# Kernel tuning notes

Hardware: AMD Instinct MI355X
Metric: run time of the kernel (lower is better)

The kernel has to match this reference:

```python
import jax, jax.numpy as jnp
import numpy as np

B, D, T, K = 16, 512, 4096, 1024

def setup_inputs() -> dict:
    key = jax.random.key(0)
    kx, kc = jax.random.split(key)
    x = jax.random.normal(kx, (B, D, T), dtype=jnp.float32)
    codebook = jax.random.normal(kc, (K, D), dtype=jnp.float32)
    return {"x": x, "codebook": codebook}

def reference(x, codebook):
    # x: [B, D, T] -> xt: [B, T, D]
    xt = jnp.transpose(x, (0, 2, 1))
    x_sq = jnp.sum(xt * xt, axis=-1, keepdims=True)          # [B, T, 1]
    c_sq = jnp.sum(codebook * codebook, axis=-1)             # [K]
    cross = jnp.einsum('btd,kd->btk', xt, codebook)          # [B, T, K]
    dist = x_sq - 2.0 * cross + c_sq                         # [B, T, K]
    indexes = jnp.argmin(dist, axis=2)                       # [B, T] int
    quantized = codebook[indexes]                            # [B, T, D]
    quantized = jnp.transpose(quantized, (0, 2, 1))          # [B, D, T]
    return quantized, indexes
```

## Files before the change

### kernel.cpp

```cpp
#include <hip/hip_runtime.h>

#define BB 16
#define DD 512
#define TT 4096
#define KK 1024

typedef _Float16 h16;
typedef __attribute__((ext_vector_type(8))) _Float16 half8;
typedef __attribute__((ext_vector_type(4))) float float4v;

#define XTH_OFF 0ull
#define XTL_OFF 67108864ull
#define CBH_OFF 134217728ull
#define CBL_OFF 135266304ull
#define CSQ_OFF 136314880ull
#define WS_NEED (136314880ull + 4096ull)

#define GLOAD_LDS16(g, l) __builtin_amdgcn_global_load_lds( \
    (const __attribute__((address_space(1))) void*)(g),      \
    (__attribute__((address_space(3))) void*)(l), 16, 0, 0)

__global__ void csq_kernel(const float* __restrict__ cb, float* __restrict__ csq) {
    int wave = threadIdx.x >> 6;
    int lane = threadIdx.x & 63;
    int row  = blockIdx.x * 4 + wave;
    const float* r = cb + (size_t)row * DD;
    float s = 0.f;
    #pragma unroll
    for (int i = 0; i < DD / 64; ++i) { float v = r[lane + i * 64]; s += v * v; }
    #pragma unroll
    for (int off = 32; off; off >>= 1) s += __shfl_down(s, off, 64);
    if (lane == 0) csq[row] = s;
}

__global__ __launch_bounds__(256) void split_x_kernel(const float* __restrict__ x,
                                                      h16* __restrict__ xth,
                                                      h16* __restrict__ xtl) {
    __shared__ float xs[32][132];
    const int tb = blockIdx.x, dcb = blockIdx.y, b = blockIdx.z;
    const int tid = threadIdx.x;
    const int t0 = tb * 128, d0 = dcb * 32;
    const float* xp = x + ((size_t)b * DD + d0) * TT + t0;
    #pragma unroll
    for (int j = 0; j < 4; ++j) {
        int i4 = tid + 256 * j;
        int dd = i4 >> 5, c4 = (i4 & 31) << 2;
        *(float4*)&xs[dd][c4] = *(const float4*)(xp + (size_t)dd * TT + c4);
    }
    __syncthreads();
    const int r = tid >> 1;
    const int ch = (tid & 1) * 16;
    h16 hv[16], lv[16];
    #pragma unroll
    for (int i = 0; i < 16; ++i) {
        float v = xs[ch + i][r];
        h16 h = (h16)v;
        hv[i] = h;
        lv[i] = (h16)(v - (float)h);
    }
    size_t o = (((size_t)(b * 32 + tb) * 16) + dcb) * 4096 + (size_t)tid * 16;
    *(half8*)(xth + o)     = *(half8*)&hv[0];
    *(half8*)(xth + o + 8) = *(half8*)&hv[8];
    *(half8*)(xtl + o)     = *(half8*)&lv[0];
    *(half8*)(xtl + o + 8) = *(half8*)&lv[8];
}

__global__ __launch_bounds__(256) void split_cb_kernel(const float* __restrict__ cb,
                                                       h16* __restrict__ cbh,
                                                       h16* __restrict__ cbl) {
    const int kb = blockIdx.x >> 4, dcb = blockIdx.x & 15;
    const int tid = threadIdx.x;
    const float* cp = cb + ((size_t)kb * 128) * DD + dcb * 32;
    h16* oh = cbh + ((size_t)(kb * 16 + dcb)) * 4096;
    h16* ol = cbl + ((size_t)(kb * 16 + dcb)) * 4096;
    #pragma unroll
    for (int j = 0; j < 4; ++j) {
        int i4 = tid + 256 * j;
        int rr = i4 >> 3, c4 = (i4 & 7) << 2;
        float4 v = *(const float4*)(cp + (size_t)rr * DD + c4);
        float vv[4] = {v.x, v.y, v.z, v.w};
        h16 h[4], l[4];
        #pragma unroll
        for (int i = 0; i < 4; ++i) {
            h[i] = (h16)vv[i];
            l[i] = (h16)(vv[i] - (float)h[i]);
        }
        *(ushort4*)(oh + rr * 32 + c4) = *(ushort4*)h;
        *(ushort4*)(ol + rr * 32 + c4) = *(ushort4*)l;
    }
}

__global__ __launch_bounds__(256, 3) void mfma_argmin_kernel(
    const h16* __restrict__ xth, const h16* __restrict__ xtl,
    const h16* __restrict__ cbh, const h16* __restrict__ cbl,
    const float* __restrict__ csq, const float* __restrict__ cb,
    float* __restrict__ idx_f_out, float* __restrict__ out) {

    __shared__ h16 ash[4096];
    __shared__ h16 asl[4096];
    __shared__ h16 bsh[4096];
    __shared__ h16 bsl[4096];
    __shared__ float redv[2][128];
    __shared__ int   redi[2][128];

    const int tid = threadIdx.x;
    const int wid = tid >> 6, lane = tid & 63;
    const int wm = wid & 1, wn = wid >> 1;
    const int tb = blockIdx.x, b = blockIdx.y;
    const int t0 = tb * 128;
    const int c  = lane & 15;
    const int q  = lane >> 4;

    const h16* aH = xth + ((size_t)(b * 32 + tb) * 16) * 4096;
    const h16* aL = xtl + ((size_t)(b * 32 + tb) * 16) * 4096;

    float best[16];
    int   bidx[16];
    #pragma unroll
    for (int i = 0; i < 16; ++i) { best[i] = 3.4e38f; bidx[i] = 0; }

    for (int kci = 0; kci < 8; ++kci) {
        const h16* bH = cbh + (size_t)kci * 16 * 4096;
        const h16* bL = cbl + (size_t)kci * 16 * 4096;
        float4v acc[4][4];
        #pragma unroll
        for (int m = 0; m < 4; ++m)
            #pragma unroll
            for (int n = 0; n < 4; ++n)
                acc[m][n] = (float4v){0.f, 0.f, 0.f, 0.f};

        for (int dcb = 0; dcb < 16; ++dcb) {
            __syncthreads();
            #pragma unroll
            for (int j = 0; j < 2; ++j) {
                int off = (tid + 256 * j) * 8;
                GLOAD_LDS16(aH + (size_t)dcb * 4096 + off, ash + off);
                GLOAD_LDS16(aL + (size_t)dcb * 4096 + off, asl + off);
                GLOAD_LDS16(bH + (size_t)dcb * 4096 + off, bsh + off);
                GLOAD_LDS16(bL + (size_t)dcb * 4096 + off, bsl + off);
            }
            __syncthreads();

            const int doff = q * 8;
            half8 Ah[4], Al[4];
            #pragma unroll
            for (int m = 0; m < 4; ++m) {
                int row = wm * 64 + m * 16 + c;
                Ah[m] = *(const half8*)(ash + row * 32 + doff);
                Al[m] = *(const half8*)(asl + row * 32 + doff);
            }
            #pragma unroll
            for (int n = 0; n < 4; ++n) {
                int row = wn * 64 + n * 16 + c;
                half8 Bh = *(const half8*)(bsh + row * 32 + doff);
                half8 Bl = *(const half8*)(bsl + row * 32 + doff);
                #pragma unroll
                for (int m = 0; m < 4; ++m) {
                    acc[m][n] = __builtin_amdgcn_mfma_f32_16x16x32_f16(Ah[m], Bh, acc[m][n], 0, 0, 0);
                    acc[m][n] = __builtin_amdgcn_mfma_f32_16x16x32_f16(Ah[m], Bl, acc[m][n], 0, 0, 0);
                    acc[m][n] = __builtin_amdgcn_mfma_f32_16x16x32_f16(Al[m], Bh, acc[m][n], 0, 0, 0);
                }
            }
        }
        #pragma unroll
        for (int n = 0; n < 4; ++n) {
            int kg = kci * 128 + wn * 64 + n * 16 + c;
            float cq = csq[kg];
            #pragma unroll
            for (int m = 0; m < 4; ++m)
                #pragma unroll
                for (int r = 0; r < 4; ++r) {
                    float s = fmaf(-2.0f, acc[m][n][r], cq);
                    int slot = m * 4 + r;
                    if (s < best[slot]) { best[slot] = s; bidx[slot] = kg; }
                }
        }
    }

    #pragma unroll
    for (int slot = 0; slot < 16; ++slot) {
        float v = best[slot]; int i = bidx[slot];
        #pragma unroll
        for (int d = 1; d < 16; d <<= 1) {
            float pv = __shfl_xor(v, d);
            int   pi = __shfl_xor(i, d);
            if (pv < v || (pv == v && pi < i)) { v = pv; i = pi; }
        }
        if (c == 0) {
            int m = slot >> 2, r = slot & 3;
            int tl = wm * 64 + m * 16 + q * 4 + r;
            redv[wn][tl] = v; redi[wn][tl] = i;
        }
    }
    __syncthreads();
    if (tid < 128) {
        float v0 = redv[0][tid]; int i0 = redi[0][tid];
        float v1 = redv[1][tid]; int i1 = redi[1][tid];
        if (v1 < v0 || (v1 == v0 && i1 < i0)) { v0 = v1; i0 = i1; }
        idx_f_out[(size_t)b * TT + t0 + tid] = (float)i0;
        redi[0][tid] = i0;
    }
    __syncthreads();

    const int tl = tid & 127, dg = tid >> 7;
    const int k = redi[0][tl];
    const float* row = cb + (size_t)k * DD + dg * 256;
    float* ob = out + ((size_t)b * DD + dg * 256) * TT + t0 + tl;
    #pragma unroll 4
    for (int i = 0; i < 64; ++i) {
        float4 v = *(const float4*)(row + i * 4);
        ob[(size_t)(i * 4 + 0) * TT] = v.x;
        ob[(size_t)(i * 4 + 1) * TT] = v.y;
        ob[(size_t)(i * 4 + 2) * TT] = v.z;
        ob[(size_t)(i * 4 + 3) * TT] = v.w;
    }
}

__global__ void gather_kernel(const float* __restrict__ cb,
                              const float* __restrict__ idx_f,
                              float* __restrict__ out) {
    int b  = blockIdx.y;
    int t  = blockIdx.x * 256 + threadIdx.x;
    int d0 = blockIdx.z * (DD / 4);
    int k  = (int)idx_f[(size_t)b * TT + t];
    const float* row = cb + (size_t)k * DD;
    float* ob = out + (size_t)b * DD * TT + t;
    #pragma unroll 8
    for (int d = d0; d < d0 + DD / 4; ++d)
        ob[(size_t)d * TT] = row[d];
}

__global__ __launch_bounds__(256) void argmin_fp32_kernel(
    const float* __restrict__ x, const float* __restrict__ cb,
    const float* __restrict__ csq, float* __restrict__ idx_f_out) {

    __shared__ float xs[32][128];
    __shared__ float cs[32][132];

    const int tid = threadIdx.x;
    const int b = blockIdx.y;
    const int t_blk = blockIdx.x * 128;
    const int tq = tid & 15, kq = tid >> 4;
    const int t0 = tq * 8, k0 = kq * 8;
    const float* xb = x + (size_t)b * DD * TT;

    float best[8]; int bidx[8];
    #pragma unroll
    for (int i = 0; i < 8; ++i) { best[i] = 3.4e38f; bidx[i] = 0; }

    for (int kc = 0; kc < KK; kc += 128) {
        float acc[8][8];
        #pragma unroll
        for (int i = 0; i < 8; ++i)
            #pragma unroll
            for (int j = 0; j < 8; ++j) acc[i][j] = 0.f;
        for (int dc = 0; dc < DD; dc += 32) {
            __syncthreads();
            #pragma unroll
            for (int j = 0; j < 4; ++j) {
                int i4 = tid + 256 * j;
                int dd = i4 >> 5, tp = (i4 & 31) << 2;
                *(float4*)&xs[dd][tp] =
                    *(const float4*)(xb + (size_t)(dc + dd) * TT + t_blk + tp);
            }
            #pragma unroll
            for (int j = 0; j < 4; ++j) {
                int i4 = tid + 256 * j;
                int kk = i4 >> 3, dq = (i4 & 7) << 2;
                float4 v = *(const float4*)(cb + (size_t)(kc + kk) * DD + dc + dq);
                cs[dq + 0][kk] = v.x; cs[dq + 1][kk] = v.y;
                cs[dq + 2][kk] = v.z; cs[dq + 3][kk] = v.w;
            }
            __syncthreads();
            #pragma unroll 8
            for (int dd = 0; dd < 32; ++dd) {
                float a[8], bv[8];
                *(float4*)&a[0]  = *(const float4*)&xs[dd][t0];
                *(float4*)&a[4]  = *(const float4*)&xs[dd][t0 + 4];
                *(float4*)&bv[0] = *(const float4*)&cs[dd][k0];
                *(float4*)&bv[4] = *(const float4*)&cs[dd][k0 + 4];
                #pragma unroll
                for (int i = 0; i < 8; ++i)
                    #pragma unroll
                    for (int j = 0; j < 8; ++j)
                        acc[i][j] = fmaf(a[i], bv[j], acc[i][j]);
            }
        }
        #pragma unroll
        for (int j = 0; j < 8; ++j) {
            int kg = kc + k0 + j;
            float cq = csq[kg];
            #pragma unroll
            for (int i = 0; i < 8; ++i) {
                float s = cq - 2.0f * acc[i][j];
                if (s < best[i]) { best[i] = s; bidx[i] = kg; }
            }
        }
    }
    __syncthreads();
    float* rbest = &xs[0][0];
    int*   ridx  = (int*)&cs[0][0];
    #pragma unroll
    for (int i = 0; i < 8; ++i) {
        rbest[kq * 128 + t0 + i] = best[i];
        ridx [kq * 128 + t0 + i] = bidx[i];
    }
    __syncthreads();
    if (tid < 128) {
        float bv = rbest[tid]; int bi = ridx[tid];
        #pragma unroll
        for (int g = 1; g < 16; ++g) {
            float v = rbest[g * 128 + tid]; int ii = ridx[g * 128 + tid];
            if (v < bv || (v == bv && ii < bi)) { bv = v; bi = ii; }
        }
        idx_f_out[(size_t)b * TT + t_blk + tid] = (float)bi;
    }
}

extern "C" void kernel_launch(void* const* d_in, const int* in_sizes, int n_in,
                              void* d_out, int out_size, void* d_ws, size_t ws_size,
                              hipStream_t stream) {
    const float* x  = (const float*)d_in[0];
    const float* cb = (const float*)d_in[1];
    float* out   = (float*)d_out;
    float* idx_f = out + (size_t)BB * DD * TT;

    if (ws_size >= WS_NEED) {
        h16* xth = (h16*)((char*)d_ws + XTH_OFF);
        h16* xtl = (h16*)((char*)d_ws + XTL_OFF);
        h16* cbh = (h16*)((char*)d_ws + CBH_OFF);
        h16* cbl = (h16*)((char*)d_ws + CBL_OFF);
        float* csq = (float*)((char*)d_ws + CSQ_OFF);

        csq_kernel<<<KK / 4, 256, 0, stream>>>(cb, csq);
        split_cb_kernel<<<128, 256, 0, stream>>>(cb, cbh, cbl);
        split_x_kernel<<<dim3(TT / 128, DD / 32, BB), 256, 0, stream>>>(x, xth, xtl);
        mfma_argmin_kernel<<<dim3(TT / 128, BB), 256, 0, stream>>>(
            xth, xtl, cbh, cbl, csq, cb, idx_f, out);
    } else {
        float* csq = (float*)d_ws;
        csq_kernel<<<KK / 4, 256, 0, stream>>>(cb, csq);
        argmin_fp32_kernel<<<dim3(TT / 128, BB), 256, 0, stream>>>(x, cb, csq, idx_f);
        gather_kernel<<<dim3(TT / 256, BB, 4), 256, 0, stream>>>(cb, idx_f, out);
    }
}
```

Measured before the change: 484.7 us.

## Double-buffer LDS tiles with async prefetch and reorder MFMA issue

Switches the A/B shared-memory tiles to two buffers and issues the global-to-LDS loads for the next (kci, dcb) step before computing on the current one, with a single waitcnt+barrier per step instead of two syncthreads. The loop over codebook chunks and D blocks is flattened into one 128-step stream so the prefetch crosses chunk boundaries. MFMAs are regrouped into three independent passes over all 16 accumulators, issued at raised wave priority. Doubling LDS use and lowering launch bounds from 3 to 2 blocks per CU cut occupancy and may raise register pressure.

```diff
diff --git a/kernel.cpp b/kernel.cpp
--- a/kernel.cpp
+++ b/kernel.cpp
@@ -90,16 +90,16 @@
     }
 }
 
-__global__ __launch_bounds__(256, 3) void mfma_argmin_kernel(
+__global__ __launch_bounds__(256, 2) void mfma_argmin_kernel(
     const h16* __restrict__ xth, const h16* __restrict__ xtl,
     const h16* __restrict__ cbh, const h16* __restrict__ cbl,
     const float* __restrict__ csq, const float* __restrict__ cb,
     float* __restrict__ idx_f_out, float* __restrict__ out) {
 
-    __shared__ h16 ash[4096];
-    __shared__ h16 asl[4096];
-    __shared__ h16 bsh[4096];
-    __shared__ h16 bsl[4096];
+    __shared__ h16 ash[2][4096];
+    __shared__ h16 asl[2][4096];
+    __shared__ h16 bsh[2][4096];
+    __shared__ h16 bsl[2][4096];
     __shared__ float redv[2][128];
     __shared__ int   redi[2][128];
 
@@ -114,14 +114,26 @@
     const h16* aH = xth + ((size_t)(b * 32 + tb) * 16) * 4096;
     const h16* aL = xtl + ((size_t)(b * 32 + tb) * 16) * 4096;
 
+    const int soff0 = tid * 8;
+    const int soff1 = soff0 + 2048;
+
+    GLOAD_LDS16(aH + soff0,  &ash[0][soff0]);
+    GLOAD_LDS16(aH + soff1,  &ash[0][soff1]);
+    GLOAD_LDS16(aL + soff0,  &asl[0][soff0]);
+    GLOAD_LDS16(aL + soff1,  &asl[0][soff1]);
+    GLOAD_LDS16(cbh + soff0, &bsh[0][soff0]);
+    GLOAD_LDS16(cbh + soff1, &bsh[0][soff1]);
+    GLOAD_LDS16(cbl + soff0, &bsl[0][soff0]);
+    GLOAD_LDS16(cbl + soff1, &bsl[0][soff1]);
+
     float best[16];
     int   bidx[16];
     #pragma unroll
     for (int i = 0; i < 16; ++i) { best[i] = 3.4e38f; bidx[i] = 0; }
 
+    asm volatile("s_waitcnt vmcnt(0)\n\ts_barrier" ::: "memory");
+
     for (int kci = 0; kci < 8; ++kci) {
-        const h16* bH = cbh + (size_t)kci * 16 * 4096;
-        const h16* bL = cbl + (size_t)kci * 16 * 4096;
         float4v acc[4][4];
         #pragma unroll
         for (int m = 0; m < 4; ++m)
@@ -130,38 +142,63 @@
                 acc[m][n] = (float4v){0.f, 0.f, 0.f, 0.f};
 
         for (int dcb = 0; dcb < 16; ++dcb) {
-            __syncthreads();
-            #pragma unroll
-            for (int j = 0; j < 2; ++j) {
-                int off = (tid + 256 * j) * 8;
-                GLOAD_LDS16(aH + (size_t)dcb * 4096 + off, ash + off);
-                GLOAD_LDS16(aL + (size_t)dcb * 4096 + off, asl + off);
-                GLOAD_LDS16(bH + (size_t)dcb * 4096 + off, bsh + off);
-                GLOAD_LDS16(bL + (size_t)dcb * 4096 + off, bsl + off);
-            }
-            __syncthreads();
+            const int g  = kci * 16 + dcb;
+            const int bf = g & 1;
+
+            if (g + 1 < 128) {
+                const int gn = g + 1;
+                const int kn = gn >> 4, dn = gn & 15;
+                const int nb = bf ^ 1;
+                const h16* aHs = aH + (size_t)dn * 4096;
+                const h16* aLs = aL + (size_t)dn * 4096;
+                const h16* bHs = cbh + ((size_t)(kn * 16 + dn)) * 4096;
+                const h16* bLs = cbl + ((size_t)(kn * 16 + dn)) * 4096;
+                GLOAD_LDS16(aHs + soff0, &ash[nb][soff0]);
+                GLOAD_LDS16(aHs + soff1, &ash[nb][soff1]);
+                GLOAD_LDS16(aLs + soff0, &asl[nb][soff0]);
+                GLOAD_LDS16(aLs + soff1, &asl[nb][soff1]);
+                GLOAD_LDS16(bHs + soff0, &bsh[nb][soff0]);
+                GLOAD_LDS16(bHs + soff1, &bsh[nb][soff1]);
+                GLOAD_LDS16(bLs + soff0, &bsl[nb][soff0]);
+                GLOAD_LDS16(bLs + soff1, &bsl[nb][soff1]);
+            }
 
             const int doff = q * 8;
-            half8 Ah[4], Al[4];
+            half8 Ah[4], Al[4], Bh[4], Bl[4];
             #pragma unroll
             for (int m = 0; m < 4; ++m) {
                 int row = wm * 64 + m * 16 + c;
-                Ah[m] = *(const half8*)(ash + row * 32 + doff);
-                Al[m] = *(const half8*)(asl + row * 32 + doff);
+                Ah[m] = *(const half8*)(&ash[bf][row * 32 + doff]);
+                Al[m] = *(const half8*)(&asl[bf][row * 32 + doff]);
             }
             #pragma unroll
             for (int n = 0; n < 4; ++n) {
                 int row = wn * 64 + n * 16 + c;
-                half8 Bh = *(const half8*)(bsh + row * 32 + doff);
-                half8 Bl = *(const half8*)(bsl + row * 32 + doff);
-                #pragma unroll
-                for (int m = 0; m < 4; ++m) {
-                    acc[m][n] = __builtin_amdgcn_mfma_f32_16x16x32_f16(Ah[m], Bh, acc[m][n], 0, 0, 0);
-                    acc[m][n] = __builtin_amdgcn_mfma_f32_16x16x32_f16(Ah[m], Bl, acc[m][n], 0, 0, 0);
-                    acc[m][n] = __builtin_amdgcn_mfma_f32_16x16x32_f16(Al[m], Bh, acc[m][n], 0, 0, 0);
-                }
-            }
-        }
+                Bh[n] = *(const half8*)(&bsh[bf][row * 32 + doff]);
+                Bl[n] = *(const half8*)(&bsl[bf][row * 32 + doff]);
+            }
+
+            __builtin_amdgcn_s_setprio(1);
+            #pragma unroll
+            for (int n = 0; n < 4; ++n)
+                #pragma unroll
+                for (int m = 0; m < 4; ++m)
+                    acc[m][n] = __builtin_amdgcn_mfma_f32_16x16x32_f16(Ah[m], Bh[n], acc[m][n], 0, 0, 0);
+            #pragma unroll
+            for (int n = 0; n < 4; ++n)
+                #pragma unroll
+                for (int m = 0; m < 4; ++m)
+                    acc[m][n] = __builtin_amdgcn_mfma_f32_16x16x32_f16(Ah[m], Bl[n], acc[m][n], 0, 0, 0);
+            #pragma unroll
+            for (int n = 0; n < 4; ++n)
+                #pragma unroll
+                for (int m = 0; m < 4; ++m)
+                    acc[m][n] = __builtin_amdgcn_mfma_f32_16x16x32_f16(Al[m], Bh[n], acc[m][n], 0, 0, 0);
+            __builtin_amdgcn_s_setprio(0);
+
+            asm volatile("s_waitcnt vmcnt(0)\n\ts_barrier" ::: "memory");
+        }
+
         #pragma unroll
         for (int n = 0; n < 4; ++n) {
             int kg = kci * 128 + wn * 64 + n * 16 + c;
```

New measurement: 501.4 us. 1.03x slower.

## Replace LDS staging with direct register double-buffered loads and 512-thread blocks

Applied to the files above, without the earlier changes.

Drops the shared-memory staging and its two barriers per d-chunk in the MFMA argmin kernel. Each wave now loads its A and B fragments straight from global memory into registers, double-buffered so the next chunk's loads overlap the current chunk's MFMAs. Blocks grow to 512 threads, each covering 256 codebook columns per fold (4 folds instead of 8), with a 4-way cross-wave reduction and a gather split across 4 groups. The cost is much higher register pressure from two fragment sets, and the same data is fetched redundantly by several waves with no LDS reuse, so the kernel leans on cache bandwidth instead.

```diff
diff --git a/kernel.cpp b/kernel.cpp
--- a/kernel.cpp
+++ b/kernel.cpp
@@ -15,10 +15,6 @@
 #define CBL_OFF 135266304ull
 #define CSQ_OFF 136314880ull
 #define WS_NEED (136314880ull + 4096ull)
-
-#define GLOAD_LDS16(g, l) __builtin_amdgcn_global_load_lds( \
-    (const __attribute__((address_space(1))) void*)(g),      \
-    (__attribute__((address_space(3))) void*)(l), 16, 0, 0)
 
 __global__ void csq_kernel(const float* __restrict__ cb, float* __restrict__ csq) {
     int wave = threadIdx.x >> 6;
@@ -90,22 +86,19 @@
     }
 }
 
-__global__ __launch_bounds__(256, 3) void mfma_argmin_kernel(
+__global__ __launch_bounds__(512, 2) void mfma_argmin_kernel(
     const h16* __restrict__ xth, const h16* __restrict__ xtl,
     const h16* __restrict__ cbh, const h16* __restrict__ cbl,
     const float* __restrict__ csq, const float* __restrict__ cb,
     float* __restrict__ idx_f_out, float* __restrict__ out) {
 
-    __shared__ h16 ash[4096];
-    __shared__ h16 asl[4096];
-    __shared__ h16 bsh[4096];
-    __shared__ h16 bsl[4096];
-    __shared__ float redv[2][128];
-    __shared__ int   redi[2][128];
+    __shared__ float redv[4][128];
+    __shared__ int   redi[4][128];
 
     const int tid = threadIdx.x;
     const int wid = tid >> 6, lane = tid & 63;
-    const int wm = wid & 1, wn = wid >> 1;
+    const int wm = wid & 1;
+    const int wn = wid >> 1;
     const int tb = blockIdx.x, b = blockIdx.y;
     const int t0 = tb * 128;
     const int c  = lane & 15;
@@ -114,68 +107,107 @@
     const h16* aH = xth + ((size_t)(b * 32 + tb) * 16) * 4096;
     const h16* aL = xtl + ((size_t)(b * 32 + tb) * 16) * 4096;
 
+    int abase[4], bbase[4];
+    #pragma unroll
+    for (int m = 0; m < 4; ++m)
+        abase[m] = (wm * 64 + m * 16 + c) * 32 + q * 8;
+    #pragma unroll
+    for (int n = 0; n < 4; ++n) {
+        int krow = wn * 64 + n * 16;
+        int hi = krow >> 7;
+        int lo = (krow & 127) + c;
+        bbase[n] = hi * 65536 + lo * 32 + q * 8;
+    }
+
     float best[16];
     int   bidx[16];
     #pragma unroll
     for (int i = 0; i < 16; ++i) { best[i] = 3.4e38f; bidx[i] = 0; }
 
-    for (int kci = 0; kci < 8; ++kci) {
-        const h16* bH = cbh + (size_t)kci * 16 * 4096;
-        const h16* bL = cbl + (size_t)kci * 16 * 4096;
-        float4v acc[4][4];
-        #pragma unroll
-        for (int m = 0; m < 4; ++m)
-            #pragma unroll
-            for (int n = 0; n < 4; ++n)
-                acc[m][n] = (float4v){0.f, 0.f, 0.f, 0.f};
-
-        for (int dcb = 0; dcb < 16; ++dcb) {
-            __syncthreads();
-            #pragma unroll
-            for (int j = 0; j < 2; ++j) {
-                int off = (tid + 256 * j) * 8;
-                GLOAD_LDS16(aH + (size_t)dcb * 4096 + off, ash + off);
-                GLOAD_LDS16(aL + (size_t)dcb * 4096 + off, asl + off);
-                GLOAD_LDS16(bH + (size_t)dcb * 4096 + off, bsh + off);
-                GLOAD_LDS16(bL + (size_t)dcb * 4096 + off, bsl + off);
-            }
-            __syncthreads();
-
-            const int doff = q * 8;
-            half8 Ah[4], Al[4];
-            #pragma unroll
-            for (int m = 0; m < 4; ++m) {
-                int row = wm * 64 + m * 16 + c;
-                Ah[m] = *(const half8*)(ash + row * 32 + doff);
-                Al[m] = *(const half8*)(asl + row * 32 + doff);
-            }
-            #pragma unroll
-            for (int n = 0; n < 4; ++n) {
-                int row = wn * 64 + n * 16 + c;
-                half8 Bh = *(const half8*)(bsh + row * 32 + doff);
-                half8 Bl = *(const half8*)(bsl + row * 32 + doff);
-                #pragma unroll
-                for (int m = 0; m < 4; ++m) {
-                    acc[m][n] = __builtin_amdgcn_mfma_f32_16x16x32_f16(Ah[m], Bh, acc[m][n], 0, 0, 0);
-                    acc[m][n] = __builtin_amdgcn_mfma_f32_16x16x32_f16(Ah[m], Bl, acc[m][n], 0, 0, 0);
-                    acc[m][n] = __builtin_amdgcn_mfma_f32_16x16x32_f16(Al[m], Bh, acc[m][n], 0, 0, 0);
-                }
-            }
-        }
-        #pragma unroll
-        for (int n = 0; n < 4; ++n) {
-            int kg = kci * 128 + wn * 64 + n * 16 + c;
-            float cq = csq[kg];
-            #pragma unroll
-            for (int m = 0; m < 4; ++m)
-                #pragma unroll
-                for (int r = 0; r < 4; ++r) {
-                    float s = fmaf(-2.0f, acc[m][n][r], cq);
-                    int slot = m * 4 + r;
-                    if (s < best[slot]) { best[slot] = s; bidx[slot] = kg; }
-                }
-        }
-    }
+    float4v acc[4][4];
+    #pragma unroll
+    for (int m = 0; m < 4; ++m)
+        #pragma unroll
+        for (int n = 0; n < 4; ++n)
+            acc[m][n] = (float4v){0.f, 0.f, 0.f, 0.f};
+
+    half8 Ah0[4], Al0[4], Bh0[4], Bl0[4];
+    half8 Ah1[4], Al1[4], Bh1[4], Bl1[4];
+
+#define LOADSET(GI, S) do {                                                  \
+        const size_t ao_ = (size_t)((GI) & 15) * 4096;                       \
+        const size_t bo_ = (size_t)((GI) >> 4) * 131072 + ao_;               \
+        _Pragma("unroll")                                                    \
+        for (int m_ = 0; m_ < 4; ++m_) {                                     \
+            Ah##S[m_] = *(const half8*)(aH + ao_ + abase[m_]);               \
+            Al##S[m_] = *(const half8*)(aL + ao_ + abase[m_]);               \
+        }                                                                    \
+        _Pragma("unroll")                                                    \
+        for (int n_ = 0; n_ < 4; ++n_) {                                     \
+            Bh##S[n_] = *(const half8*)(cbh + bo_ + bbase[n_]);              \
+            Bl##S[n_] = *(const half8*)(cbl + bo_ + bbase[n_]);              \
+        }                                                                    \
+    } while (0)
+
+#define MFMASET(S) do {                                                      \
+        _Pragma("unroll")                                                    \
+        for (int n_ = 0; n_ < 4; ++n_)                                       \
+            _Pragma("unroll")                                                \
+            for (int m_ = 0; m_ < 4; ++m_)                                   \
+                acc[m_][n_] = __builtin_amdgcn_mfma_f32_16x16x32_f16(        \
+                    Ah##S[m_], Bh##S[n_], acc[m_][n_], 0, 0, 0);             \
+        _Pragma("unroll")                                                    \
+        for (int n_ = 0; n_ < 4; ++n_)                                       \
+            _Pragma("unroll")                                                \
+            for (int m_ = 0; m_ < 4; ++m_)                                   \
+                acc[m_][n_] = __builtin_amdgcn_mfma_f32_16x16x32_f16(        \
+                    Ah##S[m_], Bl##S[n_], acc[m_][n_], 0, 0, 0);             \
+        _Pragma("unroll")                                                    \
+        for (int n_ = 0; n_ < 4; ++n_)                                       \
+            _Pragma("unroll")                                                \
+            for (int m_ = 0; m_ < 4; ++m_)                                   \
+                acc[m_][n_] = __builtin_amdgcn_mfma_f32_16x16x32_f16(        \
+                    Al##S[m_], Bh##S[n_], acc[m_][n_], 0, 0, 0);             \
+    } while (0)
+
+#define FOLD(KCI) do {                                                       \
+        _Pragma("unroll")                                                    \
+        for (int n_ = 0; n_ < 4; ++n_) {                                     \
+            int kg_ = (KCI) * 256 + wn * 64 + n_ * 16 + c;                   \
+            float cq_ = csq[kg_];                                            \
+            _Pragma("unroll")                                                \
+            for (int m_ = 0; m_ < 4; ++m_)                                   \
+                _Pragma("unroll")                                            \
+                for (int r_ = 0; r_ < 4; ++r_) {                             \
+                    float s_ = fmaf(-2.0f, acc[m_][n_][r_], cq_);            \
+                    int slot_ = m_ * 4 + r_;                                 \
+                    if (s_ < best[slot_]) { best[slot_] = s_; bidx[slot_] = kg_; } \
+                }                                                            \
+        }                                                                    \
+        _Pragma("unroll")                                                    \
+        for (int m_ = 0; m_ < 4; ++m_)                                       \
+            _Pragma("unroll")                                                \
+            for (int n_ = 0; n_ < 4; ++n_)                                   \
+                acc[m_][n_] = (float4v){0.f, 0.f, 0.f, 0.f};                 \
+    } while (0)
+
+    LOADSET(0, 0);
+    for (int gp = 0; gp < 31; ++gp) {
+        const int gi = gp * 2;
+        LOADSET(gi + 1, 1);
+        MFMASET(0);
+        LOADSET(gi + 2, 0);
+        MFMASET(1);
+        if ((gp & 7) == 7) FOLD(gp >> 3);
+    }
+    LOADSET(63, 1);
+    MFMASET(0);
+    MFMASET(1);
+    FOLD(3);
+
+#undef LOADSET
+#undef MFMASET
+#undef FOLD
 
     #pragma unroll
     for (int slot = 0; slot < 16; ++slot) {
@@ -195,8 +227,11 @@
     __syncthreads();
     if (tid < 128) {
         float v0 = redv[0][tid]; int i0 = redi[0][tid];
-        float v1 = redv[1][tid]; int i1 = redi[1][tid];
-        if (v1 < v0 || (v1 == v0 && i1 < i0)) { v0 = v1; i0 = i1; }
+        #pragma unroll
+        for (int gi = 1; gi < 4; ++gi) {
+            float v1 = redv[gi][tid]; int i1 = redi[gi][tid];
+            if (v1 < v0 || (v1 == v0 && i1 < i0)) { v0 = v1; i0 = i1; }
+        }
         idx_f_out[(size_t)b * TT + t0 + tid] = (float)i0;
         redi[0][tid] = i0;
     }
@@ -204,10 +239,10 @@
 
     const int tl = tid & 127, dg = tid >> 7;
     const int k = redi[0][tl];
-    const float* row = cb + (size_t)k * DD + dg * 256;
-    float* ob = out + ((size_t)b * DD + dg * 256) * TT + t0 + tl;
+    const float* row = cb + (size_t)k * DD + dg * 128;
+    float* ob = out + ((size_t)b * DD + dg * 128) * TT + t0 + tl;
     #pragma unroll 4
-    for (int i = 0; i < 64; ++i) {
+    for (int i = 0; i < 32; ++i) {
         float4 v = *(const float4*)(row + i * 4);
         ob[(size_t)(i * 4 + 0) * TT] = v.x;
         ob[(size_t)(i * 4 + 1) * TT] = v.y;
@@ -335,7 +370,7 @@
         csq_kernel<<<KK / 4, 256, 0, stream>>>(cb, csq);
         split_cb_kernel<<<128, 256, 0, stream>>>(cb, cbh, cbl);
         split_x_kernel<<<dim3(TT / 128, DD / 32, BB), 256, 0, stream>>>(x, xth, xtl);
-        mfma_argmin_kernel<<<dim3(TT / 128, BB), 256, 0, stream>>>(
+        mfma_argmin_kernel<<<dim3(TT / 128, BB), 512, 0, stream>>>(
             xth, xtl, cbh, cbl, csq, cb, idx_f, out);
     } else {
         float* csq = (float*)d_ws;
```

Result: slower. 522.8 us (+7.9%).

## Triple-buffer LDS with 8-wave 128x256 tiles and interleaved MFMA/load schedule

Applied to the files above, without the earlier changes.

Rewrites the main MFMA argmin kernel to use 512 threads (8 waves) per block with a 128x256 codebook tile. Global-to-LDS loads go into a three-stage ring buffer, and the MFMA clusters are split so LDS reads, async loads and barriers are interleaved with explicit waitcnt, setprio and sched_barrier. The aim is to hide memory latency and halve the number of A-tile reloads per codebook pass. In exchange, occupancy drops to one block per CU, LDS use rises to about 144KB, and correctness now depends on hand-counted vmcnt/lgkmcnt values.

```diff
diff --git a/kernel.cpp b/kernel.cpp
--- a/kernel.cpp
+++ b/kernel.cpp
@@ -90,22 +90,23 @@
     }
 }
 
-__global__ __launch_bounds__(256, 3) void mfma_argmin_kernel(
+__global__ __launch_bounds__(512, 1) void mfma_argmin_kernel(
     const h16* __restrict__ xth, const h16* __restrict__ xtl,
     const h16* __restrict__ cbh, const h16* __restrict__ cbl,
     const float* __restrict__ csq, const float* __restrict__ cb,
     float* __restrict__ idx_f_out, float* __restrict__ out) {
 
-    __shared__ h16 ash[4096];
-    __shared__ h16 asl[4096];
-    __shared__ h16 bsh[4096];
-    __shared__ h16 bsl[4096];
-    __shared__ float redv[2][128];
-    __shared__ int   redi[2][128];
+    __shared__ h16 ash[3][4096];
+    __shared__ h16 asl[3][4096];
+    __shared__ h16 bsh[3][8192];
+    __shared__ h16 bsl[3][8192];
+    __shared__ float redv[4][128];
+    __shared__ int   redi[4][128];
 
     const int tid = threadIdx.x;
     const int wid = tid >> 6, lane = tid & 63;
-    const int wm = wid & 1, wn = wid >> 1;
+    const int wm = wid & 1;
+    const int wn = wid >> 1;
     const int tb = blockIdx.x, b = blockIdx.y;
     const int t0 = tb * 128;
     const int c  = lane & 15;
@@ -114,68 +115,155 @@
     const h16* aH = xth + ((size_t)(b * 32 + tb) * 16) * 4096;
     const h16* aL = xtl + ((size_t)(b * 32 + tb) * 16) * 4096;
 
+    const int soff = tid * 8;
+
+    int arow[4];
+    #pragma unroll
+    for (int m = 0; m < 4; ++m) arow[m] = (wm * 64 + m * 16 + c) * 32 + q * 8;
+    const int brow0 = (wn * 64 +  0 + c) * 32 + q * 8;
+    const int brow1 = (wn * 64 + 16 + c) * 32 + q * 8;
+    const int brow2 = (wn * 64 + 32 + c) * 32 + q * 8;
+    const int brow3 = (wn * 64 + 48 + c) * 32 + q * 8;
+
+#define STAGE_A(GI2, BS) do { const int dn_ = (GI2) & 15;                     \
+        GLOAD_LDS16(aH + (size_t)dn_ * 4096 + soff, &ash[BS][soff]);          \
+        GLOAD_LDS16(aL + (size_t)dn_ * 4096 + soff, &asl[BS][soff]); } while (0)
+#define STAGE_BH(GI2, BS) do { const int dn_ = (GI2) & 15, kc_ = (GI2) >> 4;  \
+        const size_t b0_ = ((size_t)(kc_ * 32 + dn_)) * 4096;                 \
+        const size_t b1_ = ((size_t)(kc_ * 32 + 16 + dn_)) * 4096;            \
+        GLOAD_LDS16(cbh + b0_ + soff, &bsh[BS][soff]);                        \
+        GLOAD_LDS16(cbh + b1_ + soff, &bsh[BS][4096 + soff]); } while (0)
+#define STAGE_BL(GI2, BS) do { const int dn_ = (GI2) & 15, kc_ = (GI2) >> 4;  \
+        const size_t b0_ = ((size_t)(kc_ * 32 + dn_)) * 4096;                 \
+        const size_t b1_ = ((size_t)(kc_ * 32 + 16 + dn_)) * 4096;            \
+        GLOAD_LDS16(cbl + b0_ + soff, &bsl[BS][soff]);                        \
+        GLOAD_LDS16(cbl + b1_ + soff, &bsl[BS][4096 + soff]); } while (0)
+
+#define MF(a, bv, d) d = __builtin_amdgcn_mfma_f32_16x16x32_f16(a, bv, d, 0, 0, 0)
+#define CLUSTER(N, BH, BL, ACh, ACl) do {                                     \
+        MF(ACh[0], BH, acc[0][N]); MF(ACh[1], BH, acc[1][N]);                 \
+        MF(ACh[2], BH, acc[2][N]); MF(ACh[3], BH, acc[3][N]);                 \
+        MF(ACh[0], BL, acc[0][N]); MF(ACh[1], BL, acc[1][N]);                 \
+        MF(ACh[2], BL, acc[2][N]); MF(ACh[3], BL, acc[3][N]);                 \
+        MF(ACl[0], BH, acc[0][N]); MF(ACl[1], BH, acc[1][N]);                 \
+        MF(ACl[2], BH, acc[2][N]); MF(ACl[3], BH, acc[3][N]); } while (0)
+
     float best[16];
     int   bidx[16];
     #pragma unroll
     for (int i = 0; i < 16; ++i) { best[i] = 3.4e38f; bidx[i] = 0; }
 
-    for (int kci = 0; kci < 8; ++kci) {
-        const h16* bH = cbh + (size_t)kci * 16 * 4096;
-        const h16* bL = cbl + (size_t)kci * 16 * 4096;
-        float4v acc[4][4];
-        #pragma unroll
-        for (int m = 0; m < 4; ++m)
-            #pragma unroll
-            for (int n = 0; n < 4; ++n)
-                acc[m][n] = (float4v){0.f, 0.f, 0.f, 0.f};
-
-        for (int dcb = 0; dcb < 16; ++dcb) {
-            __syncthreads();
-            #pragma unroll
-            for (int j = 0; j < 2; ++j) {
-                int off = (tid + 256 * j) * 8;
-                GLOAD_LDS16(aH + (size_t)dcb * 4096 + off, ash + off);
-                GLOAD_LDS16(aL + (size_t)dcb * 4096 + off, asl + off);
-                GLOAD_LDS16(bH + (size_t)dcb * 4096 + off, bsh + off);
-                GLOAD_LDS16(bL + (size_t)dcb * 4096 + off, bsl + off);
-            }
-            __syncthreads();
-
-            const int doff = q * 8;
-            half8 Ah[4], Al[4];
-            #pragma unroll
-            for (int m = 0; m < 4; ++m) {
-                int row = wm * 64 + m * 16 + c;
-                Ah[m] = *(const half8*)(ash + row * 32 + doff);
-                Al[m] = *(const half8*)(asl + row * 32 + doff);
-            }
-            #pragma unroll
-            for (int n = 0; n < 4; ++n) {
-                int row = wn * 64 + n * 16 + c;
-                half8 Bh = *(const half8*)(bsh + row * 32 + doff);
-                half8 Bl = *(const half8*)(bsl + row * 32 + doff);
-                #pragma unroll
-                for (int m = 0; m < 4; ++m) {
-                    acc[m][n] = __builtin_amdgcn_mfma_f32_16x16x32_f16(Ah[m], Bh, acc[m][n], 0, 0, 0);
-                    acc[m][n] = __builtin_amdgcn_mfma_f32_16x16x32_f16(Ah[m], Bl, acc[m][n], 0, 0, 0);
-                    acc[m][n] = __builtin_amdgcn_mfma_f32_16x16x32_f16(Al[m], Bh, acc[m][n], 0, 0, 0);
-                }
-            }
-        }
-        #pragma unroll
-        for (int n = 0; n < 4; ++n) {
-            int kg = kci * 128 + wn * 64 + n * 16 + c;
-            float cq = csq[kg];
-            #pragma unroll
-            for (int m = 0; m < 4; ++m)
-                #pragma unroll
-                for (int r = 0; r < 4; ++r) {
-                    float s = fmaf(-2.0f, acc[m][n][r], cq);
-                    int slot = m * 4 + r;
-                    if (s < best[slot]) { best[slot] = s; bidx[slot] = kg; }
-                }
-        }
-    }
+    float4v acc[4][4];
+    #pragma unroll
+    for (int m = 0; m < 4; ++m)
+        #pragma unroll
+        for (int n = 0; n < 4; ++n)
+            acc[m][n] = (float4v){0.f, 0.f, 0.f, 0.f};
+
+    int bc = 0, bn = 1, bs = 2;
+
+    STAGE_A(0, 0); STAGE_BH(0, 0); STAGE_BL(0, 0);
+    STAGE_A(1, 1); STAGE_BH(1, 1); STAGE_BL(1, 1);
+    asm volatile("s_waitcnt vmcnt(6)" ::: "memory");
+    __builtin_amdgcn_s_barrier();
+    __builtin_amdgcn_sched_barrier(0);
+
+    half8 A0h[4], A0l[4], A1h[4], A1l[4];
+    half8 BhA, BlA, BhB, BlB;
+    #pragma unroll
+    for (int m = 0; m < 4; ++m) {
+        A0h[m] = *(const half8*)(&ash[0][arow[m]]);
+        A0l[m] = *(const half8*)(&asl[0][arow[m]]);
+    }
+    BhA = *(const half8*)(&bsh[0][brow0]);
+    BlA = *(const half8*)(&bsl[0][brow0]);
+
+#define GIBODY(GI, ACh, ACl, ANh, ANl, SG, VMMODE, RA) do {                   \
+          \
+    BhB = *(const half8*)(&bsh[bc][brow1]);                                   \
+    BlB = *(const half8*)(&bsl[bc][brow1]);                                   \
+    if (SG) STAGE_A((GI) + 2, bs);                                            \
+    __builtin_amdgcn_s_barrier();                                             \
+    __builtin_amdgcn_s_setprio(1); CLUSTER(0, BhA, BlA, ACh, ACl);            \
+    __builtin_amdgcn_s_setprio(0);                                            \
+         \
+    BhA = *(const half8*)(&bsh[bc][brow2]);                                   \
+    BlA = *(const half8*)(&bsl[bc][brow2]);                                   \
+    if (SG) STAGE_BH((GI) + 2, bs);                                           \
+    __builtin_amdgcn_s_barrier();                                             \
+    __builtin_amdgcn_s_setprio(1); CLUSTER(1, BhB, BlB, ACh, ACl);            \
+    __builtin_amdgcn_s_setprio(0);                                            \
+      \
+    if ((VMMODE) == 0)      asm volatile("s_waitcnt vmcnt(4)" ::: "memory");  \
+    else if ((VMMODE) == 1) asm volatile("s_waitcnt vmcnt(0)" ::: "memory");  \
+    __builtin_amdgcn_s_barrier();                                             \
+    __builtin_amdgcn_sched_barrier(0);                                        \
+    if (SG) STAGE_BL((GI) + 2, bs);                                           \
+    BhB = *(const half8*)(&bsh[bc][brow3]);                                   \
+    BlB = *(const half8*)(&bsl[bc][brow3]);                                   \
+    if (RA) {                                                                 \
+        ANh[0] = *(const half8*)(&ash[bn][arow[0]]);                          \
+        ANh[1] = *(const half8*)(&ash[bn][arow[1]]);                          \
+        ANl[0] = *(const half8*)(&asl[bn][arow[0]]);                          \
+        ANl[1] = *(const half8*)(&asl[bn][arow[1]]);                          \
+    }                                                                         \
+    __builtin_amdgcn_s_setprio(1); CLUSTER(2, BhA, BlA, ACh, ACl);            \
+    __builtin_amdgcn_s_setprio(0);                                            \
+           \
+    if (RA) {                                                                 \
+        ANh[2] = *(const half8*)(&ash[bn][arow[2]]);                          \
+        ANh[3] = *(const half8*)(&ash[bn][arow[3]]);                          \
+        ANl[2] = *(const half8*)(&asl[bn][arow[2]]);                          \
+        ANl[3] = *(const half8*)(&asl[bn][arow[3]]);                          \
+        BhA = *(const half8*)(&bsh[bn][brow0]);                               \
+        BlA = *(const half8*)(&bsl[bn][brow0]);                               \
+        asm volatile("s_waitcnt lgkmcnt(6)" ::: "memory");                    \
+    }                                                                         \
+    __builtin_amdgcn_s_barrier();                                             \
+    __builtin_amdgcn_sched_barrier(0);                                        \
+    __builtin_amdgcn_s_setprio(1); CLUSTER(3, BhB, BlB, ACh, ACl);            \
+    __builtin_amdgcn_s_setprio(0);                                            \
+    { int tr_ = bc; bc = bn; bn = bs; bs = tr_; }                             \
+} while (0)
+
+#define FOLD(KCI) do {                                                        \
+        _Pragma("unroll")                                                     \
+        for (int n_ = 0; n_ < 4; ++n_) {                                      \
+            int kg_ = (KCI) * 256 + wn * 64 + n_ * 16 + c;                    \
+            float cq_ = csq[kg_];                                             \
+            _Pragma("unroll")                                                 \
+            for (int m_ = 0; m_ < 4; ++m_)                                    \
+                _Pragma("unroll")                                             \
+                for (int r_ = 0; r_ < 4; ++r_) {                              \
+                    float s_ = fmaf(-2.0f, acc[m_][n_][r_], cq_);             \
+                    int slot_ = m_ * 4 + r_;                                  \
+                    if (s_ < best[slot_]) { best[slot_] = s_; bidx[slot_] = kg_; } \
+                }                                                             \
+        }                                                                     \
+        _Pragma("unroll")                                                     \
+        for (int m_ = 0; m_ < 4; ++m_)                                        \
+            _Pragma("unroll")                                                 \
+            for (int n_ = 0; n_ < 4; ++n_)                                    \
+                acc[m_][n_] = (float4v){0.f, 0.f, 0.f, 0.f};                  \
+    } while (0)
+
+    for (int gp = 0; gp < 31; ++gp) {
+        const int gi = gp * 2;
+        GIBODY(gi,     A0h, A0l, A1h, A1l, 1, 0, 1);
+        GIBODY(gi + 1, A1h, A1l, A0h, A0l, 1, 0, 1);
+        if ((gp & 7) == 7) FOLD(gp >> 3);
+    }
+    GIBODY(62, A0h, A0l, A1h, A1l, 0, 1, 1);
+    GIBODY(63, A1h, A1l, A0h, A0l, 0, 2, 0);
+    FOLD(3);
+
+#undef GIBODY
+#undef FOLD
+#undef CLUSTER
+#undef MF
+#undef STAGE_A
+#undef STAGE_BH
+#undef STAGE_BL
 
     #pragma unroll
     for (int slot = 0; slot < 16; ++slot) {
@@ -195,8 +283,11 @@
     __syncthreads();
     if (tid < 128) {
         float v0 = redv[0][tid]; int i0 = redi[0][tid];
-        float v1 = redv[1][tid]; int i1 = redi[1][tid];
-        if (v1 < v0 || (v1 == v0 && i1 < i0)) { v0 = v1; i0 = i1; }
+        #pragma unroll
+        for (int gi = 1; gi < 4; ++gi) {
+            float v1 = redv[gi][tid]; int i1 = redi[gi][tid];
+            if (v1 < v0 || (v1 == v0 && i1 < i0)) { v0 = v1; i0 = i1; }
+        }
         idx_f_out[(size_t)b * TT + t0 + tid] = (float)i0;
         redi[0][tid] = i0;
     }
@@ -204,10 +295,10 @@
 
     const int tl = tid & 127, dg = tid >> 7;
     const int k = redi[0][tl];
-    const float* row = cb + (size_t)k * DD + dg * 256;
-    float* ob = out + ((size_t)b * DD + dg * 256) * TT + t0 + tl;
+    const float* row = cb + (size_t)k * DD + dg * 128;
+    float* ob = out + ((size_t)b * DD + dg * 128) * TT + t0 + tl;
     #pragma unroll 4
-    for (int i = 0; i < 64; ++i) {
+    for (int i = 0; i < 32; ++i) {
         float4 v = *(const float4*)(row + i * 4);
         ob[(size_t)(i * 4 + 0) * TT] = v.x;
         ob[(size_t)(i * 4 + 1) * TT] = v.y;
@@ -335,7 +426,7 @@
         csq_kernel<<<KK / 4, 256, 0, stream>>>(cb, csq);
         split_cb_kernel<<<128, 256, 0, stream>>>(cb, cbh, cbl);
         split_x_kernel<<<dim3(TT / 128, DD / 32, BB), 256, 0, stream>>>(x, xth, xtl);
-        mfma_argmin_kernel<<<dim3(TT / 128, BB), 256, 0, stream>>>(
+        mfma_argmin_kernel<<<dim3(TT / 128, BB), 512, 0, stream>>>(
             xth, xtl, cbh, cbl, csq, cb, idx_f, out);
     } else {
         float* csq = (float*)d_ws;
```

Result: no change. 484.6 us (-0.0%).
